# Performance work log

Measured on AMD Instinct MI355X. Metric: run time of the kernel, lower is better.

## Reference

```python
import jax, jax.numpy as jnp
import numpy as np

B, LX, LM, D = 4, 512, 512, 256

def setup_inputs() -> dict:
    key = jax.random.key(0)
    ks = jax.random.split(key, 7)
    s = 1.0 / np.sqrt(D)
    return {
        "x": jax.random.normal(ks[0], (B, LX, D), jnp.float32),
        "memory": jax.random.normal(ks[1], (B, LM, D), jnp.float32),
        "memory_mask": jax.random.randint(ks[2], (B, LM), 0, 2, jnp.int32),
        "W1": jax.random.normal(ks[3], (D, D), jnp.float32) * s,
        "b1": jax.random.normal(ks[4], (D,), jnp.float32) * s,
        "W2": jax.random.normal(ks[5], (D, D), jnp.float32) * s,
        "Wt": jax.random.normal(ks[6], (D,), jnp.float32) * s,
    }

def reference(x, memory, memory_mask, W1, b1, W2, Wt):
    # item1: (B, Lx, D); item2: (B, Lm, D)
    item1 = jnp.einsum("bxd,ed->bxe", x, W1) + b1
    item2 = jnp.einsum("bmd,ed->bme", memory, W2)
    # additive attention: tanh of broadcast sum, then reduce D to scalar logit
    item = item1[:, :, None, :] + item2[:, None, :, :]  # (B, Lx, Lm, D)
    S_logit = jnp.einsum("bxmd,d->bxm", jnp.tanh(item), Wt)
    S_logit = jnp.where(memory_mask[:, None, :] == 0, jnp.float32(-10000.0), S_logit)
    return S_logit
```

## Files before the change

kernel.cpp:

```cpp
#include <hip/hip_runtime.h>

namespace {

constexpr int B = 4, LX = 512, LM = 512, D = 256;
constexpr float KSCALE = 2.8853900817779268f;
constexpr float CLAMP = 7.5f;

typedef __attribute__((ext_vector_type(8))) short short8;
typedef __attribute__((ext_vector_type(4))) float f32x4;
typedef __attribute__((ext_vector_type(2))) float f32x2;

__device__ __forceinline__ unsigned bfbits(float f) {
    unsigned u = __float_as_uint(f);
    u += 0x7FFFu + ((u >> 16) & 1u);
    return u >> 16;
}
__device__ __forceinline__ int pack2(float a, float b) {
    return (int)(bfbits(a) | (bfbits(b) << 16));
}
__device__ __forceinline__ f32x2 up2(unsigned u) {
    f32x2 r;
    r.x = __uint_as_float(u << 16);
    r.y = __uint_as_float(u & 0xFFFF0000u);
    return r;
}
__device__ __forceinline__ unsigned permb(unsigned hi, unsigned lo, unsigned sel) {
    return __builtin_amdgcn_perm(hi, lo, sel);
}

__global__ __launch_bounds__(256) void proj_mfma(
    const float* __restrict__ x, const float* __restrict__ mem,
    const float* __restrict__ W1, const float* __restrict__ b1v,
    const float* __restrict__ W2,
    unsigned short* __restrict__ E1h, unsigned short* __restrict__ E2h)
{
    const int tid = threadIdx.x;
    const int m0c = blockIdx.x * 32;
    const int e0  = blockIdx.y * 64;
    const int z   = m0c >= 2048;
    const int r0  = z ? (m0c - 2048) : m0c;
    const float* __restrict__ A = (z ? mem : x) + (size_t)r0 * D;
    const float* __restrict__ W = z ? W2 : W1;

    __shared__ short sA[32][40];
    __shared__ short sW[64][40];

    const int wv = tid >> 6, lane = tid & 63;
    const int lr = lane & 15, quad = lane >> 4;
    const int g   = wv & 1;
    const int cg0 = (wv >> 1) * 2;
    const int srA = tid >> 3;
    const int scA = (tid & 7) * 4;

    f32x4 acc0 = {0.f, 0.f, 0.f, 0.f};
    f32x4 acc1 = {0.f, 0.f, 0.f, 0.f};

    for (int kc = 0; kc < D; kc += 32) {
        float4 av = *(const float4*)&A[(size_t)srA * D + kc + scA];
        float4 w0 = *(const float4*)&W[(size_t)(e0 + srA) * D + kc + scA];
        float4 w1 = *(const float4*)&W[(size_t)(e0 + 32 + srA) * D + kc + scA];
        __syncthreads();
        *(int2*)&sA[srA][scA]      = make_int2(pack2(av.x, av.y), pack2(av.z, av.w));
        *(int2*)&sW[srA][scA]      = make_int2(pack2(w0.x, w0.y), pack2(w0.z, w0.w));
        *(int2*)&sW[srA + 32][scA] = make_int2(pack2(w1.x, w1.y), pack2(w1.z, w1.w));
        __syncthreads();
        short8 af  = *(const short8*)&sA[g * 16 + lr][quad * 8];
        short8 bf0 = *(const short8*)&sW[cg0 * 16 + lr][quad * 8];
        short8 bf1 = *(const short8*)&sW[cg0 * 16 + 16 + lr][quad * 8];
        acc0 = __builtin_amdgcn_mfma_f32_16x16x32_bf16(af, bf0, acc0, 0, 0, 0);
        acc1 = __builtin_amdgcn_mfma_f32_16x16x32_bf16(af, bf1, acc1, 0, 0, 0);
    }

    const float bias0 = z ? 0.f : b1v[e0 + cg0 * 16 + lr];
    const float bias1 = z ? 0.f : b1v[e0 + cg0 * 16 + 16 + lr];
    const int ec0 = e0 + cg0 * 16 + lr;
#pragma unroll
    for (int reg = 0; reg < 4; ++reg) {
        const int pair = quad * 4 + reg;
        float a0 = KSCALE * (acc0[reg] + bias0);
        float a1 = KSCALE * (acc1[reg] + bias1);
        a0 = fminf(fmaxf(a0, -CLAMP), CLAMP);
        a1 = fminf(fmaxf(a1, -CLAMP), CLAMP);
        const unsigned short e0b = (unsigned short)bfbits(__builtin_amdgcn_exp2f(a0));
        const unsigned short e1b = (unsigned short)bfbits(__builtin_amdgcn_exp2f(a1));
        if (!z) {
            const size_t base = (size_t)((r0 >> 5) * 16 + pair) * 256;
            E1h[(base + ec0) * 2 + g]      = e0b;
            E1h[(base + ec0 + 16) * 2 + g] = e1b;
        } else {
            const int row = r0 + g * 16 + pair;
            E2h[(size_t)row * 256 + ec0]      = e0b;
            E2h[(size_t)row * 256 + ec0 + 16] = e1b;
        }
    }
}

__global__ __launch_bounds__(256) void compact_mask(
    const int* __restrict__ mask, int* __restrict__ cidx, int* __restrict__ cnt)
{
    const int b    = threadIdx.x >> 6;
    const int lane = threadIdx.x & 63;
    int base = 0;
    for (int c = 0; c < LM / 64; ++c) {
        const int m = c * 64 + lane;
        const bool bit = mask[b * LM + m] != 0;
        const unsigned long long bal = __ballot(bit);
        const int pre = __popcll(bal & ((1ull << lane) - 1ull));
        if (bit) cidx[b * LM + base + pre] = m;
        base += __popcll(bal);
    }
    if (lane == 0) cnt[b] = base;
}

__global__ __launch_bounds__(256) void fill_out_kernel(float4* __restrict__ out4)
{
    const int i = blockIdx.x * 256 + threadIdx.x;
    const float4 v = make_float4(-10000.f, -10000.f, -10000.f, -10000.f);
    out4[i]          = v;
    out4[i + 131072] = v;
}

__global__ __launch_bounds__(256) void tanh_score_kernel(
    const unsigned* __restrict__ E1p, const unsigned* __restrict__ E2u,
    const float* __restrict__ Wt, const int* __restrict__ cidx,
    const int* __restrict__ cnt, float* __restrict__ out)
{
    const int tid = threadIdx.x;
    const int b   = blockIdx.z;
    const int x0  = blockIdx.y * 32;
    const int bx  = blockIdx.x;
    const int count = cnt[b];
    const int xt  = (b * LX + x0) >> 5;

    __shared__ unsigned sA[16 * 132];
    __shared__ unsigned sB[16 * 132];

    const int tx = tid & 15, ty = tid >> 4;
    const int pA = tid >> 4, cA = (tid & 15) * 8;
    const int pB = tid >> 4, iB = (tid & 15);

    const unsigned* gA = E1p + (size_t)(xt * 16 + pA) * 256;

    float sumW = 0.f;
#pragma unroll
    for (int i = 0; i < 256; i += 4) {
        const float4 w = *(const float4*)&Wt[i];
        sumW += (w.x + w.y) + (w.z + w.w);
    }

    const f32x2 one2 = {1.f, 1.f};

#define SPL(s)  ((f32x2){(s), (s)})
#define FMA2(A_, B_, C_) __builtin_elementwise_fma((A_), (B_), (C_))
#define OCT(BX, accv) { \
    const f32x2 T0 = FMA2(a_[0], BX(0), one2), T1 = FMA2(a_[1], BX(1), one2); \
    const f32x2 T2 = FMA2(a_[2], BX(2), one2), T3 = FMA2(a_[3], BX(3), one2); \
    const f32x2 T4 = FMA2(a_[4], BX(4), one2), T5 = FMA2(a_[5], BX(5), one2); \
    const f32x2 T6 = FMA2(a_[6], BX(6), one2), T7 = FMA2(a_[7], BX(7), one2); \
    const f32x2 L0 = T0 * T1, L1 = T2 * T3, L2 = T4 * T5, L3 = T6 * T7;       \
    const f32x2 Q0 = L0 * L1, Q1 = L2 * L3;                                   \
    const f32x2 den = Q0 * Q1;                                                \
    const f32x2 n0 = FMA2(SPL(wv[0]), T1, SPL(wv[1]) * T0);                   \
    const f32x2 n1 = FMA2(SPL(wv[2]), T3, SPL(wv[3]) * T2);                   \
    const f32x2 n2 = FMA2(SPL(wv[4]), T5, SPL(wv[5]) * T4);                   \
    const f32x2 n3 = FMA2(SPL(wv[6]), T7, SPL(wv[7]) * T6);                   \
    const f32x2 u0 = FMA2(n0, L1, n1 * L0), u1 = FMA2(n2, L3, n3 * L2);       \
    const f32x2 N  = FMA2(u0, Q1, u1 * Q0);                                   \
    f32x2 r; r.x = __builtin_amdgcn_rcpf(den.x);                              \
             r.y = __builtin_amdgcn_rcpf(den.y);                              \
    (accv) = FMA2(N, r, (accv)); }
#define BP(i)  (p_[i])
#define BPS(i) (__builtin_shufflevector(p_[i], p_[i], 1, 0))

    for (int s = bx; s < 16; s += 8) {
        const int m0 = s * 32;
        if (m0 >= count) break;

        const int c_lo = min(m0 + pB, count - 1);
        const int c_hi = min(m0 + pB + 16, count - 1);
        const unsigned* rlo = E2u + (size_t)cidx[b * LM + c_lo] * 128;
        const unsigned* rhi = E2u + (size_t)cidx[b * LM + c_hi] * 128;

        f32x2 accs = {0.f, 0.f}, accw = {0.f, 0.f};

        for (int c = 0; c < 2; ++c) {
            const int dB = c * 128;
            const uint4 A0 = *(const uint4*)(gA + dB + cA);
            const uint4 A1 = *(const uint4*)(gA + dB + cA + 4);
            const uint4 Lo = *(const uint4*)(rlo + c * 64 + iB * 4);
            const uint4 Hi = *(const uint4*)(rhi + c * 64 + iB * 4);
            uint4 P0, P1;
            P0.x = permb(Hi.x, Lo.x, 0x05040100u); P0.y = permb(Hi.x, Lo.x, 0x07060302u);
            P0.z = permb(Hi.y, Lo.y, 0x05040100u); P0.w = permb(Hi.y, Lo.y, 0x07060302u);
            P1.x = permb(Hi.z, Lo.z, 0x05040100u); P1.y = permb(Hi.z, Lo.z, 0x07060302u);
            P1.z = permb(Hi.w, Lo.w, 0x05040100u); P1.w = permb(Hi.w, Lo.w, 0x07060302u);
            __syncthreads();
            *(uint4*)&sA[pA * 132 + cA]         = A0;
            *(uint4*)&sA[pA * 132 + cA + 4]     = A1;
            *(uint4*)&sB[pB * 132 + iB * 8]     = P0;
            *(uint4*)&sB[pB * 132 + iB * 8 + 4] = P1;
            __syncthreads();

#pragma unroll 1
            for (int d = 0; d < 128; d += 8) {
                const uint4 ua0 = *(const uint4*)&sA[ty * 132 + d];
                const uint4 ua1 = *(const uint4*)&sA[ty * 132 + d + 4];
                const uint4 ub0 = *(const uint4*)&sB[tx * 132 + d];
                const uint4 ub1 = *(const uint4*)&sB[tx * 132 + d + 4];
                const float4 w0 = *(const float4*)&Wt[dB + d];
                const float4 w1 = *(const float4*)&Wt[dB + d + 4];

                const f32x2 a_[8] = {up2(ua0.x), up2(ua0.y), up2(ua0.z), up2(ua0.w),
                                     up2(ua1.x), up2(ua1.y), up2(ua1.z), up2(ua1.w)};
                const f32x2 p_[8] = {up2(ub0.x), up2(ub0.y), up2(ub0.z), up2(ub0.w),
                                     up2(ub1.x), up2(ub1.y), up2(ub1.z), up2(ub1.w)};
                const float wv[8] = {w0.x, w0.y, w0.z, w0.w, w1.x, w1.y, w1.z, w1.w};

                OCT(BP,  accs)
                OCT(BPS, accw)
            }
        }

        const int col0 = m0 + tx, col1 = m0 + 16 + tx;
        const int xA = x0 + ty, xB = x0 + 16 + ty;
        if (col0 < count) {
            const int mo = cidx[b * LM + col0];
            out[((size_t)b * LX + xA) * LM + mo] = sumW - 2.f * accs.x;
            out[((size_t)b * LX + xB) * LM + mo] = sumW - 2.f * accw.y;
        }
        if (col1 < count) {
            const int mo = cidx[b * LM + col1];
            out[((size_t)b * LX + xA) * LM + mo] = sumW - 2.f * accw.x;
            out[((size_t)b * LX + xB) * LM + mo] = sumW - 2.f * accs.y;
        }
    }
#undef BP
#undef BPS
#undef OCT
#undef FMA2
#undef SPL
}

}

extern "C" void kernel_launch(void* const* d_in, const int* in_sizes, int n_in,
                              void* d_out, int out_size, void* d_ws, size_t ws_size,
                              hipStream_t stream)
{
    const float* x    = (const float*)d_in[0];
    const float* mem  = (const float*)d_in[1];
    const int*   mask = (const int*)d_in[2];
    const float* W1   = (const float*)d_in[3];
    const float* b1   = (const float*)d_in[4];
    const float* W2   = (const float*)d_in[5];
    const float* Wt   = (const float*)d_in[6];
    float* out = (float*)d_out;

    unsigned*       E1p = (unsigned*)d_ws;
    unsigned short* E2h = (unsigned short*)(E1p + (size_t)(B * LX / 32) * 16 * 256);
    int* cidx = (int*)((char*)d_ws + 2u * 1024u * 1024u);
    int* cnt  = cidx + B * LM;

    fill_out_kernel<<<512, 256, 0, stream>>>((float4*)out);
    compact_mask<<<1, 256, 0, stream>>>(mask, cidx, cnt);
    proj_mfma<<<dim3(128, 4), 256, 0, stream>>>(
        x, mem, W1, b1, W2, (unsigned short*)E1p, E2h);
    tanh_score_kernel<<<dim3(8, 16, 4), 256, 0, stream>>>(
        E1p, (const unsigned*)E2h, Wt, cidx, cnt, out);
}
```

Baseline: 105.7 us.

## Fuse mask compaction and masked fill into tanh score kernel with split-D reduction

Drops the separate fill and mask-compaction launches. Each score block now compacts the mask into shared memory itself and writes -10000 only to the masked columns. The score kernel also splits the D dimension across two thread halves, each taking 128 features, and combines the halves through shared memory. It loads the full E1 tile once instead of per chunk and doubles the grid in y to raise parallelism. The cost is redundant mask scans in every block, an extra reduction barrier, and more shared memory per block.

```diff
diff --git a/kernel.cpp b/kernel.cpp
--- a/kernel.cpp
+++ b/kernel.cpp
@@ -45,10 +45,10 @@
     __shared__ short sA[32][40];
     __shared__ short sW[64][40];
 
-    const int wv = tid >> 6, lane = tid & 63;
+    const int wid = tid >> 6, lane = tid & 63;
     const int lr = lane & 15, quad = lane >> 4;
-    const int g   = wv & 1;
-    const int cg0 = (wv >> 1) * 2;
+    const int g   = wid & 1;
+    const int cg0 = (wid >> 1) * 2;
     const int srA = tid >> 3;
     const int scA = (tid & 7) * 4;
 
@@ -95,51 +95,58 @@
     }
 }
 
-__global__ __launch_bounds__(256) void compact_mask(
-    const int* __restrict__ mask, int* __restrict__ cidx, int* __restrict__ cnt)
-{
-    const int b    = threadIdx.x >> 6;
-    const int lane = threadIdx.x & 63;
-    int base = 0;
-    for (int c = 0; c < LM / 64; ++c) {
-        const int m = c * 64 + lane;
-        const bool bit = mask[b * LM + m] != 0;
-        const unsigned long long bal = __ballot(bit);
-        const int pre = __popcll(bal & ((1ull << lane) - 1ull));
-        if (bit) cidx[b * LM + base + pre] = m;
-        base += __popcll(bal);
-    }
-    if (lane == 0) cnt[b] = base;
-}
-
-__global__ __launch_bounds__(256) void fill_out_kernel(float4* __restrict__ out4)
-{
-    const int i = blockIdx.x * 256 + threadIdx.x;
-    const float4 v = make_float4(-10000.f, -10000.f, -10000.f, -10000.f);
-    out4[i]          = v;
-    out4[i + 131072] = v;
-}
-
-__global__ __launch_bounds__(256) void tanh_score_kernel(
+constexpr int RS = 268;
+constexpr int C1 = 136;
+
+__global__ __launch_bounds__(256, 4) void tanh_score_kernel(
     const unsigned* __restrict__ E1p, const unsigned* __restrict__ E2u,
-    const float* __restrict__ Wt, const int* __restrict__ cidx,
-    const int* __restrict__ cnt, float* __restrict__ out)
+    const float* __restrict__ Wt, const int* __restrict__ mask,
+    float* __restrict__ out)
 {
     const int tid = threadIdx.x;
     const int b   = blockIdx.z;
-    const int x0  = blockIdx.y * 32;
+    const int yb  = blockIdx.y;
+    const int T   = yb >> 1;
+    const int p0  = (yb & 1) * 8;
     const int bx  = blockIdx.x;
-    const int count = cnt[b];
-    const int xt  = (b * LX + x0) >> 5;
-
-    __shared__ unsigned sA[16 * 132];
-    __shared__ unsigned sB[16 * 132];
-
-    const int tx = tid & 15, ty = tid >> 4;
-    const int pA = tid >> 4, cA = (tid & 15) * 8;
-    const int pB = tid >> 4, iB = (tid & 15);
-
-    const unsigned* gA = E1p + (size_t)(xt * 16 + pA) * 256;
+
+    __shared__ unsigned sA[8 * RS];
+    __shared__ unsigned sB[16 * RS];
+    __shared__ int scid[LM];
+    __shared__ int smsk[LM];
+    __shared__ float4 sRed[128];
+
+    const int lane = tid & 63;
+    const int wid  = tid >> 6;
+
+    int mvv[8];
+#pragma unroll
+    for (int c = 0; c < 8; ++c) mvv[c] = mask[b * LM + c * 64 + lane];
+    int count = 0, mcount = 0;
+#pragma unroll
+    for (int c = 0; c < 8; ++c) {
+        const bool bit = mvv[c] != 0;
+        const unsigned long long bal = __ballot(bit);
+        const unsigned long long lt  = (1ull << lane) - 1ull;
+        const int pre  = __popcll(bal & lt);
+        const int prem = __popcll(~bal & lt);
+        if (wid == 0) {
+            if (bit) scid[count + pre]   = c * 64 + lane;
+            else     smsk[mcount + prem] = c * 64 + lane;
+        }
+        const int pc = __popcll(bal);
+        count  += pc;
+        mcount += 64 - pc;
+    }
+
+    {
+        const int rA = tid >> 5, q2 = tid & 31;
+        const unsigned* g =
+            E1p + (size_t)((b * 16 + T) * 16 + p0 + rA) * 256 + q2 * 8;
+        const int off = rA * RS + q2 * 8 + (q2 >= 16 ? 8 : 0);
+        *(uint4*)&sA[off]     = *(const uint4*)(g);
+        *(uint4*)&sA[off + 4] = *(const uint4*)(g + 4);
+    }
 
     float sumW = 0.f;
 #pragma unroll
@@ -148,6 +155,13 @@
         sumW += (w.x + w.y) + (w.z + w.w);
     }
 
+    __syncthreads();
+
+    const int tx = tid & 15;
+    const int ty = (tid >> 4) & 7;
+    const int h  = tid >> 7;
+    const int hb = h * 128;
+    const int ho = h * C1;
     const f32x2 one2 = {1.f, 1.f};
 
 #define SPL(s)  ((f32x2){(s), (s)})
@@ -176,62 +190,69 @@
         const int m0 = s * 32;
         if (m0 >= count) break;
 
-        const int c_lo = min(m0 + pB, count - 1);
-        const int c_hi = min(m0 + pB + 16, count - 1);
-        const unsigned* rlo = E2u + (size_t)cidx[b * LM + c_lo] * 128;
-        const unsigned* rhi = E2u + (size_t)cidx[b * LM + c_hi] * 128;
+        {
+            const int rB = tid >> 4, q = tid & 15;
+            const int clo = min(m0 + rB, count - 1);
+            const int chi = min(m0 + rB + 16, count - 1);
+            const unsigned* rlo = E2u + (size_t)(b * LM + scid[clo]) * 128 + q * 8;
+            const unsigned* rhi = E2u + (size_t)(b * LM + scid[chi]) * 128 + q * 8;
+            const uint4 Lo0 = *(const uint4*)(rlo);
+            const uint4 Lo1 = *(const uint4*)(rlo + 4);
+            const uint4 Hi0 = *(const uint4*)(rhi);
+            const uint4 Hi1 = *(const uint4*)(rhi + 4);
+            const int ob = rB * RS + q * 16 + (q >= 8 ? 8 : 0);
+            uint4 P;
+            P.x = permb(Hi0.x, Lo0.x, 0x05040100u); P.y = permb(Hi0.x, Lo0.x, 0x07060302u);
+            P.z = permb(Hi0.y, Lo0.y, 0x05040100u); P.w = permb(Hi0.y, Lo0.y, 0x07060302u);
+            *(uint4*)&sB[ob] = P;
+            P.x = permb(Hi0.z, Lo0.z, 0x05040100u); P.y = permb(Hi0.z, Lo0.z, 0x07060302u);
+            P.z = permb(Hi0.w, Lo0.w, 0x05040100u); P.w = permb(Hi0.w, Lo0.w, 0x07060302u);
+            *(uint4*)&sB[ob + 4] = P;
+            P.x = permb(Hi1.x, Lo1.x, 0x05040100u); P.y = permb(Hi1.x, Lo1.x, 0x07060302u);
+            P.z = permb(Hi1.y, Lo1.y, 0x05040100u); P.w = permb(Hi1.y, Lo1.y, 0x07060302u);
+            *(uint4*)&sB[ob + 8] = P;
+            P.x = permb(Hi1.z, Lo1.z, 0x05040100u); P.y = permb(Hi1.z, Lo1.z, 0x07060302u);
+            P.z = permb(Hi1.w, Lo1.w, 0x05040100u); P.w = permb(Hi1.w, Lo1.w, 0x07060302u);
+            *(uint4*)&sB[ob + 12] = P;
+        }
+        __syncthreads();
 
         f32x2 accs = {0.f, 0.f}, accw = {0.f, 0.f};
-
-        for (int c = 0; c < 2; ++c) {
-            const int dB = c * 128;
-            const uint4 A0 = *(const uint4*)(gA + dB + cA);
-            const uint4 A1 = *(const uint4*)(gA + dB + cA + 4);
-            const uint4 Lo = *(const uint4*)(rlo + c * 64 + iB * 4);
-            const uint4 Hi = *(const uint4*)(rhi + c * 64 + iB * 4);
-            uint4 P0, P1;
-            P0.x = permb(Hi.x, Lo.x, 0x05040100u); P0.y = permb(Hi.x, Lo.x, 0x07060302u);
-            P0.z = permb(Hi.y, Lo.y, 0x05040100u); P0.w = permb(Hi.y, Lo.y, 0x07060302u);
-            P1.x = permb(Hi.z, Lo.z, 0x05040100u); P1.y = permb(Hi.z, Lo.z, 0x07060302u);
-            P1.z = permb(Hi.w, Lo.w, 0x05040100u); P1.w = permb(Hi.w, Lo.w, 0x07060302u);
-            __syncthreads();
-            *(uint4*)&sA[pA * 132 + cA]         = A0;
-            *(uint4*)&sA[pA * 132 + cA + 4]     = A1;
-            *(uint4*)&sB[pB * 132 + iB * 8]     = P0;
-            *(uint4*)&sB[pB * 132 + iB * 8 + 4] = P1;
-            __syncthreads();
-
 #pragma unroll 1
-            for (int d = 0; d < 128; d += 8) {
-                const uint4 ua0 = *(const uint4*)&sA[ty * 132 + d];
-                const uint4 ua1 = *(const uint4*)&sA[ty * 132 + d + 4];
-                const uint4 ub0 = *(const uint4*)&sB[tx * 132 + d];
-                const uint4 ub1 = *(const uint4*)&sB[tx * 132 + d + 4];
-                const float4 w0 = *(const float4*)&Wt[dB + d];
-                const float4 w1 = *(const float4*)&Wt[dB + d + 4];
-
-                const f32x2 a_[8] = {up2(ua0.x), up2(ua0.y), up2(ua0.z), up2(ua0.w),
-                                     up2(ua1.x), up2(ua1.y), up2(ua1.z), up2(ua1.w)};
-                const f32x2 p_[8] = {up2(ub0.x), up2(ub0.y), up2(ub0.z), up2(ub0.w),
-                                     up2(ub1.x), up2(ub1.y), up2(ub1.z), up2(ub1.w)};
-                const float wv[8] = {w0.x, w0.y, w0.z, w0.w, w1.x, w1.y, w1.z, w1.w};
-
-                OCT(BP,  accs)
-                OCT(BPS, accw)
+        for (int d = 0; d < 128; d += 8) {
+            const uint4 ua0 = *(const uint4*)&sA[ty * RS + ho + d];
+            const uint4 ua1 = *(const uint4*)&sA[ty * RS + ho + d + 4];
+            const uint4 ub0 = *(const uint4*)&sB[tx * RS + ho + d];
+            const uint4 ub1 = *(const uint4*)&sB[tx * RS + ho + d + 4];
+            const float4 w0 = *(const float4*)&Wt[hb + d];
+            const float4 w1 = *(const float4*)&Wt[hb + d + 4];
+
+            const f32x2 a_[8] = {up2(ua0.x), up2(ua0.y), up2(ua0.z), up2(ua0.w),
+                                 up2(ua1.x), up2(ua1.y), up2(ua1.z), up2(ua1.w)};
+            const f32x2 p_[8] = {up2(ub0.x), up2(ub0.y), up2(ub0.z), up2(ub0.w),
+                                 up2(ub1.x), up2(ub1.y), up2(ub1.z), up2(ub1.w)};
+            const float wv[8] = {w0.x, w0.y, w0.z, w0.w, w1.x, w1.y, w1.z, w1.w};
+
+            OCT(BP,  accs)
+            OCT(BPS, accw)
+        }
+
+        if (h) sRed[ty * 16 + tx] = make_float4(accs.x, accs.y, accw.x, accw.y);
+        __syncthreads();
+        if (!h) {
+            const float4 r = sRed[ty * 16 + tx];
+            const int xA = T * 32 + p0 + ty, xB = xA + 16;
+            const int col0 = m0 + tx, col1 = m0 + 16 + tx;
+            if (col0 < count) {
+                const int mo = scid[col0];
+                out[((size_t)b * LX + xA) * LM + mo] = sumW - 2.f * (accs.x + r.x);
+                out[((size_t)b * LX + xB) * LM + mo] = sumW - 2.f * (accw.y + r.w);
             }
-        }
-
-        const int col0 = m0 + tx, col1 = m0 + 16 + tx;
-        const int xA = x0 + ty, xB = x0 + 16 + ty;
-        if (col0 < count) {
-            const int mo = cidx[b * LM + col0];
-            out[((size_t)b * LX + xA) * LM + mo] = sumW - 2.f * accs.x;
-            out[((size_t)b * LX + xB) * LM + mo] = sumW - 2.f * accw.y;
-        }
-        if (col1 < count) {
-            const int mo = cidx[b * LM + col1];
-            out[((size_t)b * LX + xA) * LM + mo] = sumW - 2.f * accw.x;
-            out[((size_t)b * LX + xB) * LM + mo] = sumW - 2.f * accs.y;
+            if (col1 < count) {
+                const int mo = scid[col1];
+                out[((size_t)b * LX + xA) * LM + mo] = sumW - 2.f * (accw.x + r.z);
+                out[((size_t)b * LX + xB) * LM + mo] = sumW - 2.f * (accs.y + r.y);
+            }
         }
     }
 #undef BP
@@ -239,6 +260,16 @@
 #undef OCT
 #undef FMA2
 #undef SPL
+
+    if (bx == 0) {
+        const int xA = T * 32 + p0 + ty, xB = xA + 16;
+        const int idx = h * 16 + tx;
+        for (int k = idx; k < mcount; k += 32) {
+            const int mo = smsk[k];
+            out[((size_t)b * LX + xA) * LM + mo] = -10000.f;
+            out[((size_t)b * LX + xB) * LM + mo] = -10000.f;
+        }
+    }
 }
 
 }
@@ -258,13 +289,10 @@
 
     unsigned*       E1p = (unsigned*)d_ws;
     unsigned short* E2h = (unsigned short*)(E1p + (size_t)(B * LX / 32) * 16 * 256);
-    int* cidx = (int*)((char*)d_ws + 2u * 1024u * 1024u);
-    int* cnt  = cidx + B * LM;
-
-    fill_out_kernel<<<512, 256, 0, stream>>>((float4*)out);
-    compact_mask<<<1, 256, 0, stream>>>(mask, cidx, cnt);
+
     proj_mfma<<<dim3(128, 4), 256, 0, stream>>>(
         x, mem, W1, b1, W2, (unsigned short*)E1p, E2h);
-    tanh_score_kernel<<<dim3(8, 16, 4), 256, 0, stream>>>(
-        E1p, (const unsigned*)E2h, Wt, cidx, cnt, out);
-}
+
+    tanh_score_kernel<<<dim3(8, 32, 4), 256, 0, stream>>>(
+        E1p, (const unsigned*)E2h, Wt, mask, out);
+}
```

After: 99.84 us. -5.5%, faster.
